# Optimization experiments

Hardware: AMD Instinct MI355X
Metric: run time of the kernel (lower is better)

Reference implementation:

```python
import jax, jax.numpy as jnp
import numpy as np

B, H, W = 8, 448, 448
HID, EMB, OUT = 1024, 1024, 4096
P = 12544
hgrid = wgrid = H // 14  # 32


def layernorm2d(x, wgt, bias, eps=1e-6):
    # channel-wise LN over dim 1 per spatial location, as in LayerNorm2d
    u = x.mean(1, keepdims=True)
    s = ((x - u) ** 2).mean(1, keepdims=True)
    x = (x - u) / jnp.sqrt(s + eps)
    return wgt[None, :, None, None] * x + bias[None, :, None, None]


def conv2d(x, wk, b, stride):
    y = jax.lax.conv_general_dilated(x, wk, (stride, stride), 'VALID',
                                     dimension_numbers=('NCHW', 'OIHW', 'NCHW'))
    return y + b[None, :, None, None]


def grid_sample_bilinear(feat, grid):
    # feat [B,C,h,w]; grid [B,P,2] (x,y) in [-1,1]; align_corners=False, zeros padding
    Bc, C, Hh, Ww = feat.shape
    gx = (grid[..., 0] + 1.0) * 0.5 * Ww - 0.5
    gy = (grid[..., 1] + 1.0) * 0.5 * Hh - 0.5
    x0 = jnp.floor(gx); y0 = jnp.floor(gy)
    x1 = x0 + 1.0; y1 = y0 + 1.0
    wx1 = gx - x0; wx0 = 1.0 - wx1
    wy1 = gy - y0; wy0 = 1.0 - wy1
    flat = feat.reshape(Bc, C, Hh * Ww)

    def gather(ix, iy):
        valid = (ix >= 0) & (ix < Ww) & (iy >= 0) & (iy < Hh)
        ixc = jnp.clip(ix, 0, Ww - 1).astype(jnp.int32)
        iyc = jnp.clip(iy, 0, Hh - 1).astype(jnp.int32)
        idx = iyc * Ww + ixc  # [B,P]
        g = jnp.take_along_axis(flat, idx[:, None, :], axis=2)  # [B,C,P]
        return g * valid[:, None, :].astype(g.dtype)

    return (gather(x0, y0) * (wx0 * wy0)[:, None, :]
            + gather(x1, y0) * (wx1 * wy0)[:, None, :]
            + gather(x0, y1) * (wx0 * wy1)[:, None, :]
            + gather(x1, y1) * (wx1 * wy1)[:, None, :])


def forward(images, masks, image_features, point_coords, valid_mask,
            c1w, c1b, ln1w, ln1b, c2w, c2b, ln2w, ln2b, c3w, c3b, up_w, up_b):
    x = jnp.concatenate([images, masks], axis=1)  # [B,4,H,W]
    x = conv2d(x, c1w, c1b, 7)
    x = jax.nn.gelu(layernorm2d(x, ln1w, ln1b), approximate=False)
    x = conv2d(x, c2w, c2b, 2)
    x = jax.nn.gelu(layernorm2d(x, ln2w, ln2b), approximate=False)
    x = conv2d(x, c3w, c3b, 1)  # [B,EMB,h,w]
    feat = image_features.reshape(B, hgrid, wgrid, EMB).transpose(0, 3, 1, 2)
    x = x + feat
    # point_sample: coords in [0,1], mapped to [-1,1]
    sf = grid_sample_bilinear(x, 2.0 * point_coords - 1.0)  # [B,EMB,P]
    sf = sf.transpose(0, 2, 1)  # [B,P,EMB]
    vm = valid_mask.astype(sf.dtype)
    pooled = (sf * vm[:, :, None]).sum(1) / vm.sum(1)[:, None]
    pooled = jnp.nan_to_num(pooled)
    out = pooled @ up_w.T + up_b  # [B,OUT]
    return out  # single feature level: stack([out]).mean(0) == out


def setup_inputs() -> dict:
    key = jax.random.key(0)
    ks = jax.random.split(key, 12)
    rng = np.random.default_rng(0)

    masks_np = np.zeros((B, 1, H, W), np.float32)
    coords = np.full((B, P, 2), -1.0, np.float32)
    valid = np.zeros((B, P), bool)
    for b in range(B):
        y0r = int(rng.integers(0, H // 2)); x0r = int(rng.integers(0, W // 2))
        hh = int(rng.integers(H // 4, H // 2)); ww = int(rng.integers(W // 4, W // 2))
        masks_np[b, 0, y0r:y0r + hh, x0r:x0r + ww] = 1.0
        ys, xs = np.nonzero(masks_np[b, 0])
        n = len(ys)
        sel = np.sort(rng.choice(n, size=min(P, n), replace=False))
        k = len(sel)
        coords[b, :k, 0] = xs[sel] / W  # x normalized (flip of (y,x))
        coords[b, :k, 1] = ys[sel] / H  # y normalized
        valid[b, :k] = True

    s = 0.02
    return {
        'images': jax.random.normal(ks[0], (B, 3, H, W), jnp.float32),
        'masks': jnp.asarray(masks_np),
        'image_features': jax.random.normal(ks[1], (B, hgrid * wgrid, EMB), jnp.float32),
        'point_coords': jnp.asarray(coords),
        'valid_mask': jnp.asarray(valid),
        'c1w': jax.random.normal(ks[2], (HID // 4, 4, 7, 7), jnp.float32) * s,
        'c1b': jnp.zeros((HID // 4,), jnp.float32),
        'ln1w': jnp.ones((HID // 4,), jnp.float32),
        'ln1b': jnp.zeros((HID // 4,), jnp.float32),
        'c2w': jax.random.normal(ks[3], (HID, HID // 4, 2, 2), jnp.float32) * s,
        'c2b': jnp.zeros((HID,), jnp.float32),
        'ln2w': jnp.ones((HID,), jnp.float32),
        'ln2b': jnp.zeros((HID,), jnp.float32),
        'c3w': jax.random.normal(ks[4], (EMB, HID, 1, 1), jnp.float32) * s,
        'c3b': jnp.zeros((EMB,), jnp.float32),
        'up_w': jax.random.normal(ks[5], (OUT, EMB), jnp.float32) * s,
        'up_b': jnp.zeros((OUT,), jnp.float32),
    }


def reference(images, masks, image_features, point_coords, valid_mask,
              c1w, c1b, ln1w, ln1b, c2w, c2b, ln2w, ln2b, c3w, c3b, up_w, up_b):
    return forward(images, masks, image_features, point_coords, valid_mask,
                   c1w, c1b, ln1w, ln1b, c2w, c2b, ln2w, ln2b, c3w, c3b, up_w, up_b)
```

## Files before the change

### kernel.cpp

```cpp
#include <hip/hip_runtime.h>
#include <stdint.h>

#define NB 8
#define HIN 448
#define CH1 256
#define CH2 1024
#define NLOC 1024
#define M2 8192
#define M1 32768
#define K1 224
#define NPTS 12544
#define NOUT 4096
#define CAP 384
#define MC (NB * CAP)
#define M1C (MC * 4)

typedef __attribute__((ext_vector_type(8))) short bf16x8;
typedef __attribute__((ext_vector_type(4))) float f32x4;

__device__ __forceinline__ short f2bf(float f) {
  uint32_t u = __builtin_bit_cast(uint32_t, f);
  uint32_t r = (u + 0x7fffu + ((u >> 16) & 1u)) >> 16;
  return (short)r;
}
__device__ __forceinline__ float bf2f(short s) {
  return __builtin_bit_cast(float, (uint32_t)(uint16_t)s << 16);
}
__device__ __forceinline__ float gelu_f(float x) {
  return 0.5f * x * (1.0f + erff(x * 0.70710678118654752f));
}
__device__ __forceinline__ void gload_lds16(const void* g, void* l) {
  __builtin_amdgcn_global_load_lds((const __attribute__((address_space(1))) unsigned int*)g,
                                   (__attribute__((address_space(3))) unsigned int*)l, 16, 0, 0);
}

__global__ void k_prep(const float* __restrict__ c1w, const float* __restrict__ c2w,
                       short* __restrict__ c1wb, short* __restrict__ w2p,
                       float4* __restrict__ zp, int n4) {
  int i = blockIdx.x * 256 + threadIdx.x;
  if (i < n4) zp[i] = make_float4(0.f, 0.f, 0.f, 0.f);
  if (i < CH1 * K1) {
    int o = i / K1, k = i - o * K1;
    int c = k / 56, kk = k - c * 56, r = kk >> 3, cc = kk & 7;
    c1wb[i] = f2bf(cc < 7 ? c1w[((o * 4 + c) * 7 + r) * 7 + cc] : 0.0f);
  }
  if (i < CH2 * CH2) {
    int o = i >> 10, k = i & 1023;
    int pos = k >> 8, ci = k & 255;
    w2p[i] = f2bf(c2w[(size_t)(o * 256 + ci) * 4 + pos]);
  }
}

__global__ __launch_bounds__(256) void k_pts(const float* __restrict__ coords,
                                             float* __restrict__ Aw,
                                             float* __restrict__ cnt,
                                             float* __restrict__ sumAw) {
  __shared__ float lAw[NLOC];
  __shared__ int lcnt;
  __shared__ float wsum[4];
  int t = threadIdx.x;
  int b = blockIdx.x / 49;
  int blk = blockIdx.x - b * 49;
  for (int i = t; i < NLOC; i += 256) lAw[i] = 0.f;
  if (t == 0) lcnt = 0;
  __syncthreads();
  int pi = blk * 256 + t;
  float x = coords[((size_t)b * NPTS + pi) * 2];
  float y = coords[((size_t)b * NPTS + pi) * 2 + 1];
  bool valid = (x >= 0.0f);
  if (valid) {
    float gx = x * 32.0f - 0.5f, gy = y * 32.0f - 0.5f;
    float x0f = floorf(gx), y0f = floorf(gy);
    int x0 = (int)x0f, y0 = (int)y0f;
    float wx1 = gx - x0f, wx0 = 1.0f - wx1;
    float wy1 = gy - y0f, wy0 = 1.0f - wy1;
    int xs[2] = {x0, x0 + 1}, ys[2] = {y0, y0 + 1};
    float wxs[2] = {wx0, wx1}, wys[2] = {wy0, wy1};
    #pragma unroll
    for (int cy = 0; cy < 2; cy++)
      #pragma unroll
      for (int cx = 0; cx < 2; cx++) {
        int ix = xs[cx], iy = ys[cy];
        if (ix >= 0 && ix < 32 && iy >= 0 && iy < 32)
          atomicAdd(&lAw[iy * 32 + ix], wxs[cx] * wys[cy]);
      }
  }
  unsigned long long ball = __ballot(valid);
  if ((t & 63) == 0) atomicAdd(&lcnt, (int)__popcll(ball));
  __syncthreads();
  float tsum = 0.f;
  for (int i = t; i < NLOC; i += 256) {
    float v = lAw[i];
    tsum += v;
    if (v != 0.f) atomicAdd(&Aw[b * NLOC + i], v);
  }
  #pragma unroll
  for (int m = 1; m <= 32; m <<= 1) tsum += __shfl_xor(tsum, m, 64);
  if ((t & 63) == 0) wsum[t >> 6] = tsum;
  __syncthreads();
  if (t == 0) {
    float bs = wsum[0] + wsum[1] + wsum[2] + wsum[3];
    if (bs != 0.f) atomicAdd(&sumAw[b], bs);
    if (lcnt) atomicAdd(&cnt[b], (float)lcnt);
  }
}

__global__ __launch_bounds__(256) void k_cim(const float* __restrict__ Aw,
                                             int* __restrict__ idxc,
                                             float* __restrict__ Awc,
                                             const float* __restrict__ images,
                                             const float* __restrict__ masks,
                                             short* __restrict__ A1g) {
  __shared__ float S[28 * 452];
  int t = threadIdx.x;
  if (blockIdx.x < NB) {
    int* cnts = (int*)S;
    int* offs = cnts + 256;
    int b = blockIdx.x;
    int base = b * 1024 + t * 4;
    float w[4];
    int c = 0;
    #pragma unroll
    for (int j = 0; j < 4; j++) { w[j] = Aw[base + j]; c += (w[j] != 0.f) ? 1 : 0; }
    cnts[t] = c;
    offs[t] = c;
    __syncthreads();
    for (int s = 1; s < 256; s <<= 1) {
      int v = (t >= s) ? offs[t - s] : 0;
      __syncthreads();
      offs[t] += v;
      __syncthreads();
    }
    int pos = b * CAP + offs[t] - cnts[t];
    int lim = (b + 1) * CAP;
    #pragma unroll
    for (int j = 0; j < 4; j++)
      if (w[j] != 0.f && pos < lim) { idxc[pos] = base + j; Awc[pos] = w[j]; pos++; }
    int total = offs[255];
    for (int i = total + t; i < CAP; i += 256) {
      idxc[b * CAP + i] = b * 1024;
      Awc[b * CAP + i] = 0.f;
    }
    return;
  }
  int bid = blockIdx.x - NB;
  int b = bid >> 6, y = bid & 63;
  int y7 = y * 7;
  for (int p = t; p < 3136; p += 256) {
    int row = p / 112, c4 = p - row * 112;
    int c = row / 7, r = row - c * 7;
    const float* src = (c < 3)
        ? &images[((size_t)(b * 3 + c) * 448 + y7 + r) * 448 + c4 * 4]
        : &masks[((size_t)b * 448 + y7 + r) * 448 + c4 * 4];
    *(float4*)&S[row * 452 + c4 * 4] = *(const float4*)src;
  }
  __syncthreads();
  size_t obase = (size_t)bid * 64 * K1;
  #pragma unroll
  for (int it = 0; it < 7; it++) {
    int p = it * 256 + t;
    int x = p / 28, k16 = p - x * 28;
    const float* s = &S[k16 * 452 + x * 7];
    short o[8];
    #pragma unroll
    for (int j = 0; j < 7; j++) o[j] = f2bf(s[j]);
    o[7] = 0;
    *(bf16x8*)&A1g[obase + (size_t)p * 8] = *(bf16x8*)o;
  }
}

template<int KDIM, int LDC, int MODE>
__global__ __launch_bounds__(256) void k_gemm64(
    const short* __restrict__ Amat, const int* __restrict__ idxc,
    const short* __restrict__ Bmat, const float* __restrict__ bias,
    short* __restrict__ Cout) {
  __shared__ __align__(16) char Lraw[16384];
  int t = threadIdx.x, lane = t & 63, wv = t >> 6;
  int mt0 = blockIdx.x * 64;
  int nt0 = blockIdx.y * 64;
  f32x4 acc[2][2];
  #pragma unroll
  for (int i = 0; i < 2; i++)
    #pragma unroll
    for (int j = 0; j < 2; j++) acc[i][j] = (f32x4){0.f, 0.f, 0.f, 0.f};

  int srow = lane >> 2, scol = (lane & 3) * 8;
  int wm = wv >> 1, wn = wv & 1;
  int l15 = lane & 15, lg = lane >> 4;

  int arow = mt0 + wv * 16 + srow;
  const short* Ap;
  if (MODE == 1) {
    int i = arow >> 2, pos = arow & 3;
    int loc = idxc[i];
    int b = loc >> 10, oy = (loc >> 5) & 31, ox = loc & 31;
    int yy = oy * 2 + (pos >> 1), xx = ox * 2 + (pos & 1);
    Ap = Amat + (size_t)((b * 64 + yy) * 64 + xx) * KDIM;
  } else {
    Ap = Amat + (size_t)arow * KDIM;
  }
  const short* Bp = Bmat + (size_t)(nt0 + wv * 16 + srow) * KDIM;

  auto STAGE = [&](int buf, int kt) {
    int k0 = kt * 32;
    char* As = Lraw + buf * 8192;
    char* Bs = As + 4096;
    gload_lds16(Ap + k0 + scol, As + wv * 1024);
    gload_lds16(Bp + k0 + scol, Bs + wv * 1024);
  };

  const int NT = KDIM / 32;
  STAGE(0, 0);
  __syncthreads();
  int cur = 0;
  #pragma unroll 2
  for (int kt = 0; kt < NT; kt++) {
    if (kt + 1 < NT) STAGE(cur ^ 1, kt + 1);
    const short* As = (const short*)(Lraw + cur * 8192);
    const short* Bs = As + 2048;
    bf16x8 af[2], bfr[2];
    #pragma unroll
    for (int i = 0; i < 2; i++)
      af[i] = *(const bf16x8*)&As[(wm * 32 + i * 16 + l15) * 32 + lg * 8];
    #pragma unroll
    for (int j = 0; j < 2; j++)
      bfr[j] = *(const bf16x8*)&Bs[(wn * 32 + j * 16 + l15) * 32 + lg * 8];
    #pragma unroll
    for (int i = 0; i < 2; i++)
      #pragma unroll
      for (int j = 0; j < 2; j++)
        acc[i][j] = __builtin_amdgcn_mfma_f32_16x16x32_bf16(af[i], bfr[j], acc[i][j], 0, 0, 0);
    __syncthreads();
    cur ^= 1;
  }

  short* ct = (short*)Lraw;
  #pragma unroll
  for (int i = 0; i < 2; i++)
    #pragma unroll
    for (int j = 0; j < 2; j++) {
      int cl = wn * 32 + j * 16 + l15;
      float bv = bias[nt0 + cl];
      #pragma unroll
      for (int reg = 0; reg < 4; reg++) {
        int rl = wm * 32 + i * 16 + lg * 4 + reg;
        ct[rl * 68 + cl] = f2bf(acc[i][j][reg] + bv);
      }
    }
  __syncthreads();
  #pragma unroll
  for (int it = 0; it < 2; it++) {
    int p = it * 256 + t;
    int row = p >> 3, cc = (p & 7) * 8;
    bf16x8 v = *(const bf16x8*)&ct[row * 68 + cc];
    *(bf16x8*)&Cout[(size_t)(mt0 + row) * LDC + nt0 + cc] = v;
  }
}

template<int KDIM>
__global__ __launch_bounds__(256) void k_gemm(
    const short* __restrict__ Amat, const short* __restrict__ Bmat,
    const float* __restrict__ bias, short* __restrict__ Cout, int ldc) {
  __shared__ __align__(16) char Lraw[24576];
  int t = threadIdx.x, lane = t & 63, wv = t >> 6;
  int mt0 = blockIdx.x * 128;
  int nt0 = blockIdx.y * 64;
  f32x4 acc[4][2];
  #pragma unroll
  for (int i = 0; i < 4; i++)
    #pragma unroll
    for (int j = 0; j < 2; j++) acc[i][j] = (f32x4){0.f, 0.f, 0.f, 0.f};

  int srow = lane >> 2, scol = (lane & 3) * 8;
  int wm = wv >> 1, wn = wv & 1;
  int l15 = lane & 15, lg = lane >> 4;
  int r0 = wv * 16, r1 = 64 + wv * 16;

  auto STAGE = [&](int buf, int kt) {
    int k0 = kt * 32;
    char* As = Lraw + buf * 12288;
    char* Bs = As + 8192;
    gload_lds16(&Amat[(size_t)(mt0 + r0 + srow) * KDIM + k0 + scol], As + r0 * 64);
    gload_lds16(&Amat[(size_t)(mt0 + r1 + srow) * KDIM + k0 + scol], As + r1 * 64);
    gload_lds16(&Bmat[(size_t)(nt0 + r0 + srow) * KDIM + k0 + scol], Bs + r0 * 64);
  };

  const int NT = KDIM / 32;
  STAGE(0, 0);
  __syncthreads();
  int cur = 0;
  #pragma unroll 2
  for (int kt = 0; kt < NT; kt++) {
    if (kt + 1 < NT) STAGE(cur ^ 1, kt + 1);
    const short* As = (const short*)(Lraw + cur * 12288);
    const short* Bs = As + 4096;
    bf16x8 af[4], bfr[2];
    #pragma unroll
    for (int i = 0; i < 4; i++)
      af[i] = *(const bf16x8*)&As[(wm * 64 + i * 16 + l15) * 32 + lg * 8];
    #pragma unroll
    for (int j = 0; j < 2; j++)
      bfr[j] = *(const bf16x8*)&Bs[(wn * 32 + j * 16 + l15) * 32 + lg * 8];
    #pragma unroll
    for (int i = 0; i < 4; i++)
      #pragma unroll
      for (int j = 0; j < 2; j++)
        acc[i][j] = __builtin_amdgcn_mfma_f32_16x16x32_bf16(af[i], bfr[j], acc[i][j], 0, 0, 0);
    __syncthreads();
    cur ^= 1;
  }

  short* ct = (short*)Lraw;
  #pragma unroll
  for (int i = 0; i < 4; i++)
    #pragma unroll
    for (int j = 0; j < 2; j++) {
      int cl = wn * 32 + j * 16 + l15;
      float bv = bias[nt0 + cl];
      #pragma unroll
      for (int reg = 0; reg < 4; reg++) {
        int rl = wm * 64 + i * 16 + lg * 4 + reg;
        ct[rl * 68 + cl] = f2bf(acc[i][j][reg] + bv);
      }
    }
  __syncthreads();
  #pragma unroll
  for (int it = 0; it < 4; it++) {
    int p = it * 256 + t;
    int row = p >> 3, cc = (p & 7) * 8;
    bf16x8 v = *(const bf16x8*)&ct[row * 68 + cc];
    *(bf16x8*)&Cout[(size_t)(mt0 + row) * ldc + nt0 + cc] = v;
  }
}

__global__ __launch_bounds__(256) void k_ln1c(const short* __restrict__ y1c,
                                              const float* __restrict__ ln1w,
                                              const float* __restrict__ ln1b,
                                              short* __restrict__ act1c) {
  int t = threadIdx.x, wv = t >> 6, lane = t & 63;
  int c = lane * 4;
  float lw[4], lb[4];
  #pragma unroll
  for (int j = 0; j < 4; j++) { lw[j] = ln1w[c + j]; lb[j] = ln1b[c + j]; }
  int j0 = blockIdx.x * 64 + wv * 16;
  for (int r = 0; r < 16; r++) {
    int j = j0 + r;
    short4 v4 = *(const short4*)&y1c[(size_t)j * 256 + c];
    float xs[4] = {bf2f(v4.x), bf2f(v4.y), bf2f(v4.z), bf2f(v4.w)};
    float s = 0.f, q = 0.f;
    #pragma unroll
    for (int jj = 0; jj < 4; jj++) { s += xs[jj]; q += xs[jj] * xs[jj]; }
    #pragma unroll
    for (int mm = 1; mm <= 32; mm <<= 1) { s += __shfl_xor(s, mm, 64); q += __shfl_xor(q, mm, 64); }
    float u = s * (1.0f / 256.0f);
    float rs = rsqrtf(q * (1.0f / 256.0f) - u * u + 1e-6f);
    short o[4];
    #pragma unroll
    for (int jj = 0; jj < 4; jj++) o[jj] = f2bf(gelu_f(lw[jj] * ((xs[jj] - u) * rs) + lb[jj]));
    size_t addr = (size_t)(j >> 2) * 1024 + (size_t)(j & 3) * 256 + c;
    *(short4*)&act1c[addr] = make_short4(o[0], o[1], o[2], o[3]);
  }
}

__global__ __launch_bounds__(256) void k_poolboth(const short* __restrict__ y2c,
                                                  const float* __restrict__ feat,
                                                  const int* __restrict__ idxc,
                                                  const float* __restrict__ ln2w,
                                                  const float* __restrict__ ln2b,
                                                  const float* __restrict__ Awc,
                                                  float* __restrict__ partials,
                                                  float* __restrict__ partialsF) {
  int t = threadIdx.x, wv = t >> 6, lane = t & 63;
  int b = blockIdx.x / 12, chunk = blockIdx.x % 12;
  int base = b * CAP + chunk * 32;
  int c0 = lane * 16;
  float lw[16], lb[16], wacc[16], facc[16];
  #pragma unroll
  for (int j = 0; j < 16; j++) {
    lw[j] = ln2w[c0 + j];
    lb[j] = ln2b[c0 + j];
    wacc[j] = 0.f;
    facc[j] = 0.f;
  }
  for (int pass = 0; pass < 8; pass++) {
    int row = base + pass * 4 + wv;
    float wt = Awc[row];
    if (wt == 0.f) continue;
    const float4* fp = (const float4*)(feat + (size_t)idxc[row] * 1024 + c0);
    #pragma unroll
    for (int j = 0; j < 4; j++) {
      float4 v = fp[j];
      facc[j * 4 + 0] += wt * v.x;
      facc[j * 4 + 1] += wt * v.y;
      facc[j * 4 + 2] += wt * v.z;
      facc[j * 4 + 3] += wt * v.w;
    }
    bf16x8 v0 = *(const bf16x8*)&y2c[(size_t)row * 1024 + c0];
    bf16x8 v1 = *(const bf16x8*)&y2c[(size_t)row * 1024 + c0 + 8];
    float xs[16];
    #pragma unroll
    for (int j = 0; j < 8; j++) { xs[j] = bf2f(v0[j]); xs[8 + j] = bf2f(v1[j]); }
    float s = 0.f, q = 0.f;
    #pragma unroll
    for (int j = 0; j < 16; j++) { s += xs[j]; q += xs[j] * xs[j]; }
    #pragma unroll
    for (int m = 1; m <= 32; m <<= 1) { s += __shfl_xor(s, m, 64); q += __shfl_xor(q, m, 64); }
    float u = s * (1.0f / 1024.0f);
    float rs = rsqrtf(q * (1.0f / 1024.0f) - u * u + 1e-6f);
    #pragma unroll
    for (int j = 0; j < 16; j++)
      wacc[j] += wt * gelu_f(lw[j] * ((xs[j] - u) * rs) + lb[j]);
  }
  float* dst = &partials[((size_t)blockIdx.x * 4 + wv) * 1024 + c0];
  float* dstF = &partialsF[((size_t)blockIdx.x * 4 + wv) * 1024 + c0];
  #pragma unroll
  for (int j = 0; j < 4; j++) {
    *(f32x4*)&dst[j * 4] = (f32x4){wacc[j * 4], wacc[j * 4 + 1], wacc[j * 4 + 2], wacc[j * 4 + 3]};
    *(f32x4*)&dstF[j * 4] = (f32x4){facc[j * 4], facc[j * 4 + 1], facc[j * 4 + 2], facc[j * 4 + 3]};
  }
}

__global__ __launch_bounds__(256) void k_red(const float* __restrict__ partials,
                                             const float* __restrict__ partialsF,
                                             float* __restrict__ pa,
                                             float* __restrict__ pf) {
  int c = blockIdx.x * 256 + threadIdx.x;
  int b = c >> 10, ch = c & 1023;
  const float* p = partials + (size_t)(b * 48) * 1024 + ch;
  const float* pF = partialsF + (size_t)(b * 48) * 1024 + ch;
  float s = 0.f, sf = 0.f;
  #pragma unroll 8
  for (int j = 0; j < 48; j++) {
    s += p[(size_t)j * 1024];
    sf += pF[(size_t)j * 1024];
  }
  pa[c] = s;
  pf[c] = sf;
}

__global__ __launch_bounds__(256) void k_mix(const float* __restrict__ pa,
                                             const float* __restrict__ pf,
                                             const float* __restrict__ sumAw,
                                             const float* __restrict__ cnt,
                                             const float* __restrict__ c3w,
                                             const float* __restrict__ c3b,
                                             float* __restrict__ zn) {
  __shared__ float pl[8192];
  int t = threadIdx.x;
  for (int idx = t; idx < 2048; idx += 256)
    ((float4*)pl)[idx] = ((const float4*)pa)[idx];
  __syncthreads();
  int wv = t >> 6, lane = t & 63;
  int c = blockIdx.x * 4 + wv;
  float w[16];
  #pragma unroll
  for (int i = 0; i < 16; i++) w[i] = c3w[(size_t)c * 1024 + i * 64 + lane];
  float s[8];
  #pragma unroll
  for (int b = 0; b < 8; b++) s[b] = 0.f;
  #pragma unroll
  for (int i = 0; i < 16; i++) {
    int k = i * 64 + lane;
    #pragma unroll
    for (int b = 0; b < 8; b++) s[b] += w[i] * pl[b * 1024 + k];
  }
  #pragma unroll
  for (int m = 1; m <= 32; m <<= 1)
    #pragma unroll
    for (int b = 0; b < 8; b++) s[b] += __shfl_xor(s[b], m, 64);
  if (lane < 8) {
    float cv = cnt[lane];
    float z = s[lane] + sumAw[lane] * c3b[c] + pf[lane * 1024 + c];
    zn[lane * 1024 + c] = cv > 0.f ? z / cv : 0.f;
  }
}

__global__ __launch_bounds__(256) void k_out(const float* __restrict__ zn,
                                             const float* __restrict__ up_w,
                                             const float* __restrict__ up_b,
                                             float* __restrict__ out) {
  __shared__ float pl[8192];
  int t = threadIdx.x;
  for (int idx = t; idx < 2048; idx += 256)
    ((float4*)pl)[idx] = ((const float4*)zn)[idx];
  __syncthreads();
  int wv = t >> 6, lane = t & 63;
  int o = blockIdx.x * 4 + wv;
  float w[16];
  #pragma unroll
  for (int i = 0; i < 16; i++) w[i] = up_w[(size_t)o * 1024 + i * 64 + lane];
  float s[8];
  #pragma unroll
  for (int b = 0; b < 8; b++) s[b] = 0.f;
  #pragma unroll
  for (int i = 0; i < 16; i++) {
    int k = i * 64 + lane;
    #pragma unroll
    for (int b = 0; b < 8; b++) s[b] += w[i] * pl[b * 1024 + k];
  }
  #pragma unroll
  for (int m = 1; m <= 32; m <<= 1)
    #pragma unroll
    for (int b = 0; b < 8; b++) s[b] += __shfl_xor(s[b], m, 64);
  if (lane < 8) out[(size_t)lane * NOUT + o] = s[lane] + up_b[o];
}

extern "C" void kernel_launch(void* const* d_in, const int* in_sizes, int n_in,
                              void* d_out, int out_size, void* d_ws, size_t ws_size,
                              hipStream_t stream) {
  const float* images = (const float*)d_in[0];
  const float* masks  = (const float*)d_in[1];
  const float* feat   = (const float*)d_in[2];
  const float* coords = (const float*)d_in[3];
  const float* c1w  = (const float*)d_in[5];
  const float* c1b  = (const float*)d_in[6];
  const float* ln1w = (const float*)d_in[7];
  const float* ln1b = (const float*)d_in[8];
  const float* c2w  = (const float*)d_in[9];
  const float* c2b  = (const float*)d_in[10];
  const float* ln2w = (const float*)d_in[11];
  const float* ln2b = (const float*)d_in[12];
  const float* c3w  = (const float*)d_in[13];
  const float* c3b  = (const float*)d_in[14];
  const float* up_w = (const float*)d_in[15];
  const float* up_b = (const float*)d_in[16];
  float* out = (float*)d_out;

  char* ws = (char*)d_ws;
  size_t off = 0;
  auto alloc = [&](size_t bytes) -> void* {
    void* p = ws + off;
    off = (off + bytes + 255) & ~(size_t)255;
    return p;
  };
  float* Aw    = (float*)alloc(8192 * 4);
  float* cnt   = (float*)alloc(8 * 4);
  float* sumAw = (float*)alloc(8 * 4);
  size_t zeroBytes = off;
  int*   idxc  = (int*)alloc(MC * 4);
  float* Awc   = (float*)alloc(MC * 4);
  float* pa    = (float*)alloc(8192 * 4);
  float* pf    = (float*)alloc(8192 * 4);
  float* partials  = (float*)alloc((size_t)384 * 1024 * 4);
  float* partialsF = (float*)alloc((size_t)384 * 1024 * 4);
  float* zn   = (float*)alloc(8192 * 4);
  short* c1wb = (short*)alloc((size_t)CH1 * K1 * 2);
  short* w2p  = (short*)alloc((size_t)CH2 * CH2 * 2);
  short* A1g  = (short*)alloc((size_t)M1 * K1 * 2);
  short* y1c  = (short*)alloc((size_t)M1C * 256 * 2);
  short* act1c = (short*)alloc((size_t)MC * 1024 * 2);
  short* y2c  = (short*)alloc((size_t)MC * 1024 * 2);

  int n4 = (int)(zeroBytes / 16);
  k_prep<<<4096, 256, 0, stream>>>(c1w, c2w, c1wb, w2p, (float4*)d_ws, n4);
  k_pts<<<NB * 49, 256, 0, stream>>>(coords, Aw, cnt, sumAw);
  k_cim<<<NB + 512, 256, 0, stream>>>(Aw, idxc, Awc, images, masks, A1g);
  k_gemm64<K1, 256, 1><<<dim3(M1C / 64, 4), 256, 0, stream>>>(A1g, idxc, c1wb, c1b, y1c);
  k_ln1c<<<M1C / 64, 256, 0, stream>>>(y1c, ln1w, ln1b, act1c);
  k_gemm<1024><<<dim3(MC / 128, 16), 256, 0, stream>>>(act1c, w2p, c2b, y2c, 1024);
  k_poolboth<<<96, 256, 0, stream>>>(y2c, feat, idxc, ln2w, ln2b, Awc, partials, partialsF);
  k_red<<<32, 256, 0, stream>>>(partials, partialsF, pa, pf);
  k_mix<<<256, 256, 0, stream>>>(pa, pf, sumAw, cnt, c3w, c3b, zn);
  k_out<<<NOUT / 4, 256, 0, stream>>>(zn, up_w, up_b, out);
}
```

Measured before the change: 112.3 us.

## Split-K the second GEMM and fuse tail kernels into one cooperative kernel

The 1024-K GEMM is split into two K halves along grid z. Each half writes fp32 partial results directly to global memory, skipping the LDS-staged bf16 epilogue. This doubles the number of blocks so more CUs get work. The pooling, reduction, c3 mixing and output projection kernels are merged into one cooperative kernel separated by grid-wide syncs, which removes three launch gaps. The cost is extra fp32 write and read traffic for two partial buffers, less coalesced stores, and the overhead of the grid barriers.

```diff
diff --git a/kernel.cpp b/kernel.cpp
--- a/kernel.cpp
+++ b/kernel.cpp
@@ -1,5 +1,8 @@
 #include <hip/hip_runtime.h>
+#include <hip/hip_cooperative_groups.h>
 #include <stdint.h>
+
+namespace cg = cooperative_groups;
 
 #define NB 8
 #define HIN 448
@@ -257,14 +260,18 @@
   }
 }
 
-template<int KDIM>
-__global__ __launch_bounds__(256) void k_gemm(
+__global__ __launch_bounds__(256) void k_gemm2s(
     const short* __restrict__ Amat, const short* __restrict__ Bmat,
-    const float* __restrict__ bias, short* __restrict__ Cout, int ldc) {
+    const float* __restrict__ bias, float* __restrict__ y2p0,
+    float* __restrict__ y2p1) {
+  const int KDIM = 1024;
   __shared__ __align__(16) char Lraw[24576];
   int t = threadIdx.x, lane = t & 63, wv = t >> 6;
   int mt0 = blockIdx.x * 128;
   int nt0 = blockIdx.y * 64;
+  int kz = blockIdx.z;
+  int kbase = kz * 512;
+  float* outp = kz ? y2p1 : y2p0;
   f32x4 acc[4][2];
   #pragma unroll
   for (int i = 0; i < 4; i++)
@@ -277,7 +284,7 @@
   int r0 = wv * 16, r1 = 64 + wv * 16;
 
   auto STAGE = [&](int buf, int kt) {
-    int k0 = kt * 32;
+    int k0 = kbase + kt * 32;
     char* As = Lraw + buf * 12288;
     char* Bs = As + 8192;
     gload_lds16(&Amat[(size_t)(mt0 + r0 + srow) * KDIM + k0 + scol], As + r0 * 64);
@@ -285,13 +292,12 @@
     gload_lds16(&Bmat[(size_t)(nt0 + r0 + srow) * KDIM + k0 + scol], Bs + r0 * 64);
   };
 
-  const int NT = KDIM / 32;
   STAGE(0, 0);
   __syncthreads();
   int cur = 0;
   #pragma unroll 2
-  for (int kt = 0; kt < NT; kt++) {
-    if (kt + 1 < NT) STAGE(cur ^ 1, kt + 1);
+  for (int kt = 0; kt < 16; kt++) {
+    if (kt + 1 < 16) STAGE(cur ^ 1, kt + 1);
     const short* As = (const short*)(Lraw + cur * 12288);
     const short* Bs = As + 4096;
     bf16x8 af[4], bfr[2];
@@ -310,27 +316,18 @@
     cur ^= 1;
   }
 
-  short* ct = (short*)Lraw;
   #pragma unroll
   for (int i = 0; i < 4; i++)
     #pragma unroll
     for (int j = 0; j < 2; j++) {
-      int cl = wn * 32 + j * 16 + l15;
-      float bv = bias[nt0 + cl];
+      int colg = nt0 + wn * 32 + j * 16 + l15;
+      float bv = kz ? 0.0f : bias[colg];
       #pragma unroll
       for (int reg = 0; reg < 4; reg++) {
-        int rl = wm * 64 + i * 16 + lg * 4 + reg;
-        ct[rl * 68 + cl] = f2bf(acc[i][j][reg] + bv);
+        int rowg = mt0 + wm * 64 + i * 16 + lg * 4 + reg;
+        outp[(size_t)rowg * 1024 + colg] = acc[i][j][reg] + bv;
       }
     }
-  __syncthreads();
-  #pragma unroll
-  for (int it = 0; it < 4; it++) {
-    int p = it * 256 + t;
-    int row = p >> 3, cc = (p & 7) * 8;
-    bf16x8 v = *(const bf16x8*)&ct[row * 68 + cc];
-    *(bf16x8*)&Cout[(size_t)(mt0 + row) * ldc + nt0 + cc] = v;
-  }
 }
 
 __global__ __launch_bounds__(256) void k_ln1c(const short* __restrict__ y1c,
@@ -357,152 +354,154 @@
     short o[4];
     #pragma unroll
     for (int jj = 0; jj < 4; jj++) o[jj] = f2bf(gelu_f(lw[jj] * ((xs[jj] - u) * rs) + lb[jj]));
-    size_t addr = (size_t)(j >> 2) * 1024 + (size_t)(j & 3) * 256 + c;
-    *(short4*)&act1c[addr] = make_short4(o[0], o[1], o[2], o[3]);
-  }
-}
-
-__global__ __launch_bounds__(256) void k_poolboth(const short* __restrict__ y2c,
-                                                  const float* __restrict__ feat,
-                                                  const int* __restrict__ idxc,
-                                                  const float* __restrict__ ln2w,
-                                                  const float* __restrict__ ln2b,
-                                                  const float* __restrict__ Awc,
-                                                  float* __restrict__ partials,
-                                                  float* __restrict__ partialsF) {
+    *(short4*)&act1c[(size_t)j * 256 + c] = make_short4(o[0], o[1], o[2], o[3]);
+  }
+}
+
+__global__ __launch_bounds__(256) void k_tail(
+    const float* __restrict__ y2p0, const float* __restrict__ y2p1,
+    const float* __restrict__ feat, const int* __restrict__ idxc,
+    const float* __restrict__ ln2w, const float* __restrict__ ln2b,
+    const float* __restrict__ Awc, float* __restrict__ partials,
+    float* __restrict__ partialsF, float* __restrict__ pa,
+    float* __restrict__ pf, const float* __restrict__ sumAw,
+    const float* __restrict__ cnt, const float* __restrict__ c3w,
+    const float* __restrict__ c3b, const float* __restrict__ up_w,
+    const float* __restrict__ up_b, float* __restrict__ zn,
+    float* __restrict__ out) {
+  cg::grid_group grid = cg::this_grid();
+  __shared__ float pl[8192];
   int t = threadIdx.x, wv = t >> 6, lane = t & 63;
-  int b = blockIdx.x / 12, chunk = blockIdx.x % 12;
-  int base = b * CAP + chunk * 32;
-  int c0 = lane * 16;
-  float lw[16], lb[16], wacc[16], facc[16];
-  #pragma unroll
-  for (int j = 0; j < 16; j++) {
-    lw[j] = ln2w[c0 + j];
-    lb[j] = ln2b[c0 + j];
-    wacc[j] = 0.f;
-    facc[j] = 0.f;
-  }
-  for (int pass = 0; pass < 8; pass++) {
-    int row = base + pass * 4 + wv;
-    float wt = Awc[row];
-    if (wt == 0.f) continue;
-    const float4* fp = (const float4*)(feat + (size_t)idxc[row] * 1024 + c0);
+
+  if (blockIdx.x < 96) {
+    int b = blockIdx.x / 12, chunk = blockIdx.x % 12;
+    int base = b * CAP + chunk * 32;
+    int c0 = lane * 16;
+    float lw[16], lb[16], wacc[16], facc[16];
+    #pragma unroll
+    for (int j = 0; j < 16; j++) {
+      lw[j] = ln2w[c0 + j];
+      lb[j] = ln2b[c0 + j];
+      wacc[j] = 0.f;
+      facc[j] = 0.f;
+    }
+    for (int pass = 0; pass < 8; pass++) {
+      int row = base + pass * 4 + wv;
+      float wt = Awc[row];
+      if (wt == 0.f) continue;
+      const float4* fp = (const float4*)(feat + (size_t)idxc[row] * 1024 + c0);
+      #pragma unroll
+      for (int j = 0; j < 4; j++) {
+        float4 v = fp[j];
+        facc[j * 4 + 0] += wt * v.x;
+        facc[j * 4 + 1] += wt * v.y;
+        facc[j * 4 + 2] += wt * v.z;
+        facc[j * 4 + 3] += wt * v.w;
+      }
+      const float4* a0 = (const float4*)(y2p0 + (size_t)row * 1024 + c0);
+      const float4* a1 = (const float4*)(y2p1 + (size_t)row * 1024 + c0);
+      float xs[16];
+      #pragma unroll
+      for (int j = 0; j < 4; j++) {
+        float4 va = a0[j], vb = a1[j];
+        xs[j * 4 + 0] = va.x + vb.x;
+        xs[j * 4 + 1] = va.y + vb.y;
+        xs[j * 4 + 2] = va.z + vb.z;
+        xs[j * 4 + 3] = va.w + vb.w;
+      }
+      float s = 0.f, q = 0.f;
+      #pragma unroll
+      for (int j = 0; j < 16; j++) { s += xs[j]; q += xs[j] * xs[j]; }
+      #pragma unroll
+      for (int m = 1; m <= 32; m <<= 1) { s += __shfl_xor(s, m, 64); q += __shfl_xor(q, m, 64); }
+      float u = s * (1.0f / 1024.0f);
+      float rs = rsqrtf(q * (1.0f / 1024.0f) - u * u + 1e-6f);
+      #pragma unroll
+      for (int j = 0; j < 16; j++)
+        wacc[j] += wt * gelu_f(lw[j] * ((xs[j] - u) * rs) + lb[j]);
+    }
+    float* dst = &partials[((size_t)blockIdx.x * 4 + wv) * 1024 + c0];
+    float* dstF = &partialsF[((size_t)blockIdx.x * 4 + wv) * 1024 + c0];
     #pragma unroll
     for (int j = 0; j < 4; j++) {
-      float4 v = fp[j];
-      facc[j * 4 + 0] += wt * v.x;
-      facc[j * 4 + 1] += wt * v.y;
-      facc[j * 4 + 2] += wt * v.z;
-      facc[j * 4 + 3] += wt * v.w;
-    }
-    bf16x8 v0 = *(const bf16x8*)&y2c[(size_t)row * 1024 + c0];
-    bf16x8 v1 = *(const bf16x8*)&y2c[(size_t)row * 1024 + c0 + 8];
-    float xs[16];
-    #pragma unroll
-    for (int j = 0; j < 8; j++) { xs[j] = bf2f(v0[j]); xs[8 + j] = bf2f(v1[j]); }
-    float s = 0.f, q = 0.f;
-    #pragma unroll
-    for (int j = 0; j < 16; j++) { s += xs[j]; q += xs[j] * xs[j]; }
-    #pragma unroll
-    for (int m = 1; m <= 32; m <<= 1) { s += __shfl_xor(s, m, 64); q += __shfl_xor(q, m, 64); }
-    float u = s * (1.0f / 1024.0f);
-    float rs = rsqrtf(q * (1.0f / 1024.0f) - u * u + 1e-6f);
-    #pragma unroll
-    for (int j = 0; j < 16; j++)
-      wacc[j] += wt * gelu_f(lw[j] * ((xs[j] - u) * rs) + lb[j]);
-  }
-  float* dst = &partials[((size_t)blockIdx.x * 4 + wv) * 1024 + c0];
-  float* dstF = &partialsF[((size_t)blockIdx.x * 4 + wv) * 1024 + c0];
-  #pragma unroll
-  for (int j = 0; j < 4; j++) {
-    *(f32x4*)&dst[j * 4] = (f32x4){wacc[j * 4], wacc[j * 4 + 1], wacc[j * 4 + 2], wacc[j * 4 + 3]};
-    *(f32x4*)&dstF[j * 4] = (f32x4){facc[j * 4], facc[j * 4 + 1], facc[j * 4 + 2], facc[j * 4 + 3]};
-  }
-}
-
-__global__ __launch_bounds__(256) void k_red(const float* __restrict__ partials,
-                                             const float* __restrict__ partialsF,
-                                             float* __restrict__ pa,
-                                             float* __restrict__ pf) {
-  int c = blockIdx.x * 256 + threadIdx.x;
-  int b = c >> 10, ch = c & 1023;
-  const float* p = partials + (size_t)(b * 48) * 1024 + ch;
-  const float* pF = partialsF + (size_t)(b * 48) * 1024 + ch;
-  float s = 0.f, sf = 0.f;
-  #pragma unroll 8
-  for (int j = 0; j < 48; j++) {
-    s += p[(size_t)j * 1024];
-    sf += pF[(size_t)j * 1024];
-  }
-  pa[c] = s;
-  pf[c] = sf;
-}
-
-__global__ __launch_bounds__(256) void k_mix(const float* __restrict__ pa,
-                                             const float* __restrict__ pf,
-                                             const float* __restrict__ sumAw,
-                                             const float* __restrict__ cnt,
-                                             const float* __restrict__ c3w,
-                                             const float* __restrict__ c3b,
-                                             float* __restrict__ zn) {
-  __shared__ float pl[8192];
-  int t = threadIdx.x;
-  for (int idx = t; idx < 2048; idx += 256)
-    ((float4*)pl)[idx] = ((const float4*)pa)[idx];
-  __syncthreads();
-  int wv = t >> 6, lane = t & 63;
-  int c = blockIdx.x * 4 + wv;
-  float w[16];
-  #pragma unroll
-  for (int i = 0; i < 16; i++) w[i] = c3w[(size_t)c * 1024 + i * 64 + lane];
-  float s[8];
-  #pragma unroll
-  for (int b = 0; b < 8; b++) s[b] = 0.f;
-  #pragma unroll
-  for (int i = 0; i < 16; i++) {
-    int k = i * 64 + lane;
-    #pragma unroll
-    for (int b = 0; b < 8; b++) s[b] += w[i] * pl[b * 1024 + k];
-  }
-  #pragma unroll
-  for (int m = 1; m <= 32; m <<= 1)
-    #pragma unroll
-    for (int b = 0; b < 8; b++) s[b] += __shfl_xor(s[b], m, 64);
-  if (lane < 8) {
-    float cv = cnt[lane];
-    float z = s[lane] + sumAw[lane] * c3b[c] + pf[lane * 1024 + c];
-    zn[lane * 1024 + c] = cv > 0.f ? z / cv : 0.f;
-  }
-}
-
-__global__ __launch_bounds__(256) void k_out(const float* __restrict__ zn,
-                                             const float* __restrict__ up_w,
-                                             const float* __restrict__ up_b,
-                                             float* __restrict__ out) {
-  __shared__ float pl[8192];
-  int t = threadIdx.x;
-  for (int idx = t; idx < 2048; idx += 256)
-    ((float4*)pl)[idx] = ((const float4*)zn)[idx];
-  __syncthreads();
-  int wv = t >> 6, lane = t & 63;
-  int o = blockIdx.x * 4 + wv;
-  float w[16];
-  #pragma unroll
-  for (int i = 0; i < 16; i++) w[i] = up_w[(size_t)o * 1024 + i * 64 + lane];
-  float s[8];
-  #pragma unroll
-  for (int b = 0; b < 8; b++) s[b] = 0.f;
-  #pragma unroll
-  for (int i = 0; i < 16; i++) {
-    int k = i * 64 + lane;
-    #pragma unroll
-    for (int b = 0; b < 8; b++) s[b] += w[i] * pl[b * 1024 + k];
-  }
-  #pragma unroll
-  for (int m = 1; m <= 32; m <<= 1)
-    #pragma unroll
-    for (int b = 0; b < 8; b++) s[b] += __shfl_xor(s[b], m, 64);
-  if (lane < 8) out[(size_t)lane * NOUT + o] = s[lane] + up_b[o];
+      *(f32x4*)&dst[j * 4] = (f32x4){wacc[j * 4], wacc[j * 4 + 1], wacc[j * 4 + 2], wacc[j * 4 + 3]};
+      *(f32x4*)&dstF[j * 4] = (f32x4){facc[j * 4], facc[j * 4 + 1], facc[j * 4 + 2], facc[j * 4 + 3]};
+    }
+  }
+  grid.sync();
+
+  if (blockIdx.x < 32) {
+    int c = blockIdx.x * 256 + t;
+    int b = c >> 10, ch = c & 1023;
+    const float* p = partials + (size_t)(b * 48) * 1024 + ch;
+    const float* pF = partialsF + (size_t)(b * 48) * 1024 + ch;
+    float s = 0.f, sf = 0.f;
+    #pragma unroll 8
+    for (int j = 0; j < 48; j++) {
+      s += p[(size_t)j * 1024];
+      sf += pF[(size_t)j * 1024];
+    }
+    pa[c] = s;
+    pf[c] = sf;
+  }
+  grid.sync();
+
+  {
+    for (int idx = t; idx < 2048; idx += 256)
+      ((float4*)pl)[idx] = ((const float4*)pa)[idx];
+    __syncthreads();
+    int c = blockIdx.x * 4 + wv;
+    float w[16];
+    #pragma unroll
+    for (int i = 0; i < 16; i++) w[i] = c3w[(size_t)c * 1024 + i * 64 + lane];
+    float s[8];
+    #pragma unroll
+    for (int b = 0; b < 8; b++) s[b] = 0.f;
+    #pragma unroll
+    for (int i = 0; i < 16; i++) {
+      int k = i * 64 + lane;
+      #pragma unroll
+      for (int b = 0; b < 8; b++) s[b] += w[i] * pl[b * 1024 + k];
+    }
+    #pragma unroll
+    for (int m = 1; m <= 32; m <<= 1)
+      #pragma unroll
+      for (int b = 0; b < 8; b++) s[b] += __shfl_xor(s[b], m, 64);
+    if (lane < 8) {
+      float cv = cnt[lane];
+      float z = s[lane] + sumAw[lane] * c3b[c] + pf[lane * 1024 + c];
+      zn[lane * 1024 + c] = cv > 0.f ? z / cv : 0.f;
+    }
+  }
+  grid.sync();
+
+  {
+    __syncthreads();
+    for (int idx = t; idx < 2048; idx += 256)
+      ((float4*)pl)[idx] = ((const float4*)zn)[idx];
+    __syncthreads();
+    #pragma unroll
+    for (int ii = 0; ii < 4; ii++) {
+      int o = blockIdx.x * 16 + wv * 4 + ii;
+      float w[16];
+      #pragma unroll
+      for (int i = 0; i < 16; i++) w[i] = up_w[(size_t)o * 1024 + i * 64 + lane];
+      float s[8];
+      #pragma unroll
+      for (int b = 0; b < 8; b++) s[b] = 0.f;
+      #pragma unroll
+      for (int i = 0; i < 16; i++) {
+        int k = i * 64 + lane;
+        #pragma unroll
+        for (int b = 0; b < 8; b++) s[b] += w[i] * pl[b * 1024 + k];
+      }
+      #pragma unroll
+      for (int m = 1; m <= 32; m <<= 1)
+        #pragma unroll
+        for (int b = 0; b < 8; b++) s[b] += __shfl_xor(s[b], m, 64);
+      if (lane < 8) out[(size_t)lane * NOUT + o] = s[lane] + up_b[o];
+    }
+  }
 }
 
 extern "C" void kernel_launch(void* const* d_in, const int* in_sizes, int n_in,
@@ -549,7 +548,8 @@
   short* A1g  = (short*)alloc((size_t)M1 * K1 * 2);
   short* y1c  = (short*)alloc((size_t)M1C * 256 * 2);
   short* act1c = (short*)alloc((size_t)MC * 1024 * 2);
-  short* y2c  = (short*)alloc((size_t)MC * 1024 * 2);
+  float* y2p0 = (float*)alloc((size_t)MC * 1024 * 4);
+  float* y2p1 = (float*)alloc((size_t)MC * 1024 * 4);
 
   int n4 = (int)(zeroBytes / 16);
   k_prep<<<4096, 256, 0, stream>>>(c1w, c2w, c1wb, w2p, (float4*)d_ws, n4);
@@ -557,9 +557,9 @@
   k_cim<<<NB + 512, 256, 0, stream>>>(Aw, idxc, Awc, images, masks, A1g);
   k_gemm64<K1, 256, 1><<<dim3(M1C / 64, 4), 256, 0, stream>>>(A1g, idxc, c1wb, c1b, y1c);
   k_ln1c<<<M1C / 64, 256, 0, stream>>>(y1c, ln1w, ln1b, act1c);
-  k_gemm<1024><<<dim3(MC / 128, 16), 256, 0, stream>>>(act1c, w2p, c2b, y2c, 1024);
-  k_poolboth<<<96, 256, 0, stream>>>(y2c, feat, idxc, ln2w, ln2b, Awc, partials, partialsF);
-  k_red<<<32, 256, 0, stream>>>(partials, partialsF, pa, pf);
-  k_mix<<<256, 256, 0, stream>>>(pa, pf, sumAw, cnt, c3w, c3b, zn);
-  k_out<<<NOUT / 4, 256, 0, stream>>>(zn, up_w, up_b, out);
-}
+  k_gemm2s<<<dim3(MC / 128, 16, 2), 256, 0, stream>>>(act1c, w2p, c2b, y2p0, y2p1);
+  void* targs[] = {&y2p0, &y2p1, (void*)&feat, &idxc, (void*)&ln2w, (void*)&ln2b,
+                   &Awc, &partials, &partialsF, &pa, &pf, &sumAw, &cnt,
+                   (void*)&c3w, (void*)&c3b, (void*)&up_w, (void*)&up_b, &zn, &out};
+  hipLaunchCooperativeKernel((void*)k_tail, dim3(256), dim3(256), targs, 0, stream);
+}
```

Result: slower. 194.5 us (+73.3%).
